# Optimization experiments

Measured on AMD Instinct MI355X. Metric: run time of the kernel, lower is better.

The kernel has to match this reference:

```python
import jax, jax.numpy as jnp
import numpy as np

N = 10000
E = 160000
B = 16
NEG_SLOPE = 0.2


def gat_conv(x, src, dst, W, a_src, a_dst, b, heads, ch):
    # x: [N, F_in]; src/dst: [E'] (self-loops included); W: [F_in, heads*ch]
    n = x.shape[0]
    h = (x @ W).reshape(n, heads, ch)                     # [N,H,C]
    alpha_src = jnp.sum(h * a_src, axis=-1)               # [N,H]
    alpha_dst = jnp.sum(h * a_dst, axis=-1)               # [N,H]
    e = jax.nn.leaky_relu(alpha_src[src] + alpha_dst[dst], NEG_SLOPE)  # [E,H]
    # segment softmax over edges grouped by destination node
    m = jax.ops.segment_max(e, dst, num_segments=n)       # [N,H]
    ex = jnp.exp(e - m[dst])                              # [E,H]
    denom = jax.ops.segment_sum(ex, dst, num_segments=n)  # [N,H]
    alpha = ex / denom[dst]                               # [E,H]
    out = jax.ops.segment_sum(alpha[:, :, None] * h[src], dst, num_segments=n)  # [N,H,C]
    return out.reshape(n, heads * ch) + b


def setup_inputs() -> dict:
    key = jax.random.key(0)
    ks = jax.random.split(key, 16)
    glorot = lambda k, shp: jax.random.normal(k, shp, jnp.float32) * np.sqrt(2.0 / (shp[0] + shp[-1]))
    inp = {
        "x": jax.random.normal(ks[0], (N, 128), jnp.float32),
        "edge_index": jax.random.randint(ks[1], (2, E), 0, N, jnp.int64),
        "batch": jnp.sort(jax.random.randint(ks[2], (N,), 0, B, jnp.int64)),
        # conv1: 128 -> 128 per head, 8 heads
        "W1": glorot(ks[3], (128, 8 * 128)),
        "att_src1": glorot(ks[4], (8, 128)),
        "att_dst1": glorot(ks[5], (8, 128)),
        "b1": jnp.zeros((8 * 128,), jnp.float32),
        # conv2: 1024 -> 64 per head, 8 heads
        "W2": glorot(ks[6], (1024, 8 * 64)),
        "att_src2": glorot(ks[7], (8, 64)),
        "att_dst2": glorot(ks[8], (8, 64)),
        "b2": jnp.zeros((8 * 64,), jnp.float32),
        "fc1_w": glorot(ks[9], (512, 32)),
        "fc1_b": jnp.zeros((32,), jnp.float32),
        "fc2_w": glorot(ks[10], (32, 10)),
        "fc2_b": jnp.zeros((10,), jnp.float32),
    }
    return inp


def reference(x, edge_index, batch, W1, att_src1, att_dst1, b1,
              W2, att_src2, att_dst2, b2, fc1_w, fc1_b, fc2_w, fc2_b):
    n = x.shape[0]
    loop = jnp.arange(n, dtype=edge_index.dtype)
    src = jnp.concatenate([edge_index[0], loop])  # PyG add_self_loops=True
    dst = jnp.concatenate([edge_index[1], loop])
    h = jax.nn.elu(gat_conv(x, src, dst, W1, att_src1, att_dst1, b1, 8, 128))   # [N,1024]
    h = jax.nn.elu(gat_conv(h, src, dst, W2, att_src2, att_dst2, b2, 8, 64))    # [N,512]
    # global mean pool over graphs
    sums = jax.ops.segment_sum(h, batch, num_segments=B)                        # [B,512]
    cnt = jax.ops.segment_sum(jnp.ones((n,), h.dtype), batch, num_segments=B)
    g = sums / jnp.maximum(cnt, 1.0)[:, None]
    g = jax.nn.elu(g @ fc1_w + fc1_b)
    return g @ fc2_w + fc2_b                                                    # [B,10]
```

## Files before the change

kernel.cpp:

```cpp
#include <hip/hip_runtime.h>
#include <math.h>

#define HEADS 8
#define NEG 0.2f

typedef unsigned short ushort_t;
typedef __attribute__((ext_vector_type(8))) short short8;
typedef float f32x4 __attribute__((ext_vector_type(4)));

__device__ inline ushort_t f2bf(float f) {
  union { float f; unsigned u; } v; v.f = f;
  unsigned r = (v.u + 0x7FFF + ((v.u >> 16) & 1)) >> 16;
  return (ushort_t)r;
}

__device__ inline float4 bf4(uint2 v) {
  union { unsigned u; float f; } a, b, c, d;
  a.u = v.x << 16; b.u = v.x & 0xffff0000u;
  c.u = v.y << 16; d.u = v.y & 0xffff0000u;
  return make_float4(a.f, b.f, c.f, d.f);
}

__device__ inline float elu_f(float v) {
  return (v > 0.f) ? v : (__expf(v) - 1.f);
}

#define GLDS16(gp, lp)                                                          \
  __builtin_amdgcn_global_load_lds(                                             \
      (const __attribute__((address_space(1))) void*)(gp),                      \
      (__attribute__((address_space(3))) void*)(lp), 16, 0, 0)

__global__ __launch_bounds__(256) void init_k(int* __restrict__ ws, int zero_words,
                                              const float* __restrict__ x,
                                              ushort_t* __restrict__ xb,
                                              const float* __restrict__ W1,
                                              ushort_t* __restrict__ w1t,
                                              const float* __restrict__ W2,
                                              ushort_t* __restrict__ w2t, int nx4) {
  __shared__ float tile[32][33];
  int blk = blockIdx.x;
  if (blk < 640) {
    const float* W; ushort_t* Wt; int K, N, tk, tn;
    if (blk < 128) { W = W1; Wt = w1t; K = 128; N = 1024; tk = blk >> 5; tn = blk & 31; }
    else { W = W2; Wt = w2t; K = 1024; N = 512; int t = blk - 128; tk = t >> 4; tn = t & 15; }
    int tx = threadIdx.x & 31, ty = threadIdx.x >> 5;
    int k0 = tk * 32, n0 = tn * 32;
#pragma unroll
    for (int r = 0; r < 4; r++)
      tile[ty + r * 8][tx] = W[(size_t)(k0 + ty + r * 8) * N + n0 + tx];
    __syncthreads();
#pragma unroll
    for (int r = 0; r < 4; r++)
      Wt[(size_t)(n0 + ty + r * 8) * K + k0 + tx] = f2bf(tile[tx][ty + r * 8]);
  } else {
    int i = (blk - 640) * 256 + threadIdx.x;
    if (i < zero_words) ws[i] = 0;
    if (i < nx4) {
      float4 v = ((const float4*)x)[i];
      ushort_t o[4] = {f2bf(v.x), f2bf(v.y), f2bf(v.z), f2bf(v.w)};
      *(uint2*)&xb[i * 4] = *(uint2*)o;
    }
  }
}

__global__ void prep_k(const int* __restrict__ ei, int* __restrict__ src,
                       int* __restrict__ dst, int* __restrict__ deg,
                       const int* __restrict__ batch, int* __restrict__ bstart,
                       int* __restrict__ bend, int E, int Nn) {
  int i = blockIdx.x * blockDim.x + threadIdx.x;
  if (i < Nn) {
    int b = batch[i];
    if (i == 0 || batch[i - 1] != b) bstart[b] = i;
    if (i == Nn - 1 || batch[i + 1] != b) bend[b] = i + 1;
  }
  if (i >= E + Nn) return;
  int s, d;
  if (i < E) { s = ei[i]; d = ei[E + i]; }
  else       { s = d = i - E; }
  src[i] = s;
  dst[i] = d;
  atomicAdd(&deg[d], 1);
}

__global__ __launch_bounds__(1024) void scan_k(const int* __restrict__ deg,
                                               int* __restrict__ offs,
                                               int* __restrict__ cursor, int Nn) {
  __shared__ int wtot[16];
  __shared__ int wexcl[16];
  __shared__ int soff_s;
  int t = threadIdx.x;
  int lane = t & 63, w = t >> 6;
  if (t == 0) soff_s = 0;
  __syncthreads();
  for (int base = 0; base < Nn; base += 4096) {
    int idx = base + 4 * t;
    int4 v = make_int4(0, 0, 0, 0);
    if (idx + 3 < Nn) v = *(const int4*)&deg[idx];
    else {
      if (idx < Nn)     v.x = deg[idx];
      if (idx + 1 < Nn) v.y = deg[idx + 1];
      if (idx + 2 < Nn) v.z = deg[idx + 2];
      if (idx + 3 < Nn) v.w = deg[idx + 3];
    }
    int s1 = v.x, s2 = s1 + v.y, s3 = s2 + v.z, s4 = s3 + v.w;
    int sc = s4;
#pragma unroll
    for (int o = 1; o < 64; o <<= 1) {
      int x = __shfl_up(sc, o);
      if (lane >= o) sc += x;
    }
    if (lane == 63) wtot[w] = sc;
    __syncthreads();
    if (w == 0) {
      int tv = (lane < 16) ? wtot[lane] : 0;
      int ts = tv;
#pragma unroll
      for (int o = 1; o < 16; o <<= 1) {
        int x = __shfl_up(ts, o);
        if (lane >= o) ts += x;
      }
      if (lane < 16) wexcl[lane] = ts - tv;
      if (lane == 15) wtot[15] = ts;
    }
    __syncthreads();
    int excl = soff_s + wexcl[w] + (sc - s4);
    int o0 = excl, o1 = excl + s1, o2 = excl + s2, o3 = excl + s3;
    if (idx < Nn)     { offs[idx] = o0;     cursor[idx] = o0; }
    if (idx + 1 < Nn) { offs[idx + 1] = o1; cursor[idx + 1] = o1; }
    if (idx + 2 < Nn) { offs[idx + 2] = o2; cursor[idx + 2] = o2; }
    if (idx + 3 < Nn) { offs[idx + 3] = o3; cursor[idx + 3] = o3; }
    int chunk_total = wtot[15];
    __syncthreads();
    if (t == 0) soff_s += chunk_total;
    __syncthreads();
  }
  if (t == 0) offs[Nn] = soff_s;
}

__global__ void scatter_k(const int* __restrict__ src, const int* __restrict__ dst,
                          int* __restrict__ cursor, int* __restrict__ psrc, int Etot) {
  int i = blockIdx.x * blockDim.x + threadIdx.x;
  if (i >= Etot) return;
  int p = atomicAdd(&cursor[dst[i]], 1);
  psrc[p] = src[i];
}

__global__ __launch_bounds__(256) void mfma_gemm_k(const ushort_t* __restrict__ A,
                                                   const ushort_t* __restrict__ Bt,
                                                   ushort_t* __restrict__ Cb,
                                                   const float* __restrict__ att_s,
                                                   const float* __restrict__ att_d,
                                                   float* __restrict__ asrc,
                                                   float* __restrict__ adst,
                                                   int M, int N, int K, int CSHIFT) {
  __shared__ __attribute__((aligned(16))) ushort_t lds[32768];
  int tid = threadIdx.x;
  int lane = tid & 63;
  int wave = tid >> 6;
  int wm = (wave >> 1) * 64, wn = (wave & 1) * 64;
  int bm = blockIdx.y * 128, bn = blockIdx.x * 128;
  int lrow = lane & 15, lq = lane >> 4;

  f32x4 acc[4][4];
#pragma unroll
  for (int i = 0; i < 4; i++)
#pragma unroll
    for (int j = 0; j < 4; j++) acc[i][j] = 0.f;

  int srow = lane >> 3;
  int scol = 8 * ((lane & 7) ^ srow);
  const ushort_t* pa[4];
  const ushort_t* pb[4];
  int lofs[4];
#pragma unroll
  for (int c = 0; c < 4; c++) {
    int row = wave * 32 + c * 8 + srow;
    int ga = min(bm + row, M - 1);
    pa[c] = &A[(size_t)ga * K + scol];
    pb[c] = &Bt[(size_t)(bn + row) * K + scol];
    lofs[c] = (wave * 4 + c) * 512;
  }

  auto stage = [&](int buf, int k0) {
#pragma unroll
    for (int c = 0; c < 4; c++) GLDS16(pa[c] + k0, &lds[buf * 8192 + lofs[c]]);
#pragma unroll
    for (int c = 0; c < 4; c++) GLDS16(pb[c] + k0, &lds[16384 + buf * 8192 + lofs[c]]);
  };

  auto compute = [&](int buf) {
    const ushort_t* Asb = &lds[buf * 8192];
    const ushort_t* Bsb = &lds[16384 + buf * 8192];
#pragma unroll
    for (int ks = 0; ks < 2; ks++) {
      short8 af[4], bfr[4];
#pragma unroll
      for (int t = 0; t < 4; t++) {
        int cbs = (ks * 64 + lq * 16) ^ ((lrow & 7) << 4);
        af[t]  = *(const short8*)&Asb[(wm + t * 16 + lrow) * 64 + (cbs >> 1)];
        bfr[t] = *(const short8*)&Bsb[(wn + t * 16 + lrow) * 64 + (cbs >> 1)];
      }
#pragma unroll
      for (int i = 0; i < 4; i++)
#pragma unroll
        for (int j = 0; j < 4; j++)
          acc[i][j] = __builtin_amdgcn_mfma_f32_16x16x32_bf16(af[i], bfr[j], acc[i][j], 0, 0, 0);
    }
  };

  int NT = K >> 6;
  stage(0, 0);
  asm volatile("s_waitcnt vmcnt(0)" ::: "memory");
  __builtin_amdgcn_s_barrier();
  int cur = 0;
  for (int t = 0; t + 1 < NT; ++t) {
    stage(cur ^ 1, (t + 1) << 6);
    compute(cur);
    asm volatile("s_waitcnt vmcnt(0)" ::: "memory");
    __builtin_amdgcn_s_barrier();
    cur ^= 1;
  }
  compute(cur);

  __syncthreads();

  ushort_t* Cl = lds;
  float* pls = (float*)&lds[17472];
  float* pld = pls + 256;

  {
    float avs[4], avd[4];
#pragma unroll
    for (int j = 0; j < 4; j++) {
      int col = bn + wn + j * 16 + lrow;
      avs[j] = att_s[col];
      avd[j] = att_d[col];
    }
#pragma unroll
    for (int i = 0; i < 4; i++) {
#pragma unroll
      for (int r = 0; r < 4; r++) {
        float ps = 0.f, pd = 0.f;
#pragma unroll
        for (int j = 0; j < 4; j++) {
          float v = acc[i][j][r];
          ps += v * avs[j];
          pd += v * avd[j];
        }
#pragma unroll
        for (int o = 1; o < 16; o <<= 1) {
          ps += __shfl_xor(ps, o);
          pd += __shfl_xor(pd, o);
        }
        if (lrow == 0) {
          int rr = i * 16 + lq * 4 + r;
          pls[wave * 64 + rr] = ps;
          pld[wave * 64 + rr] = pd;
        }
      }
    }
  }

#pragma unroll
  for (int i = 0; i < 4; i++) {
#pragma unroll
    for (int j = 0; j < 4; j++) {
      int col = wn + j * 16 + lrow;
#pragma unroll
      for (int r = 0; r < 4; r++) {
        int row = wm + i * 16 + lq * 4 + r;
        Cl[row * 136 + col] = f2bf(acc[i][j][r]);
      }
    }
  }
  __syncthreads();

#pragma unroll
  for (int p = 0; p < 8; p++) {
    int row = p * 16 + (tid >> 4);
    int col8 = (tid & 15) * 8;
    if (bm + row < M)
      *(uint4*)&Cb[(size_t)(bm + row) * N + bn + col8] = *(const uint4*)&Cl[row * 136 + col8];
  }

  {
    int r = tid & 127, half = tid >> 7;
    if (bm + r < M) {
      const float* P = half ? pld : pls;
      float* O = half ? adst : asrc;
      int w0 = (r >> 6) * 2, idx = r & 63;
      float va = P[w0 * 64 + idx];
      float vb = P[(w0 + 1) * 64 + idx];
      int h0 = bn >> CSHIFT, h1 = (bn + 64) >> CSHIFT;
      size_t base = (size_t)(bm + r) * HEADS;
      if (h0 == h1) O[base + h0] = va + vb;
      else { O[base + h0] = va; O[base + h1] = vb; }
    }
  }
}

template <int F, int CSHIFT, int BT, int NSPLIT, typename OT>
__global__ __launch_bounds__(BT) void aggregate_k(const ushort_t* __restrict__ hb,
                                                  const float* __restrict__ asrc,
                                                  const float* __restrict__ adst,
                                                  const int* __restrict__ offs,
                                                  const int* __restrict__ psrc,
                                                  const float* __restrict__ bias,
                                                  OT* __restrict__ out) {
  constexpr int CPB = F / NSPLIT;
  constexpr int G = (1 << CSHIFT) >> 2;
  static_assert(CPB == 4 * BT, "CPB/thread mismatch");
  static_assert(G >= 8 && G <= 64, "head group must cover the 8-edge batch");
  int nb = blockIdx.x;
  int n = nb / NSPLIT;
  int coff = (nb - n * NSPLIT) * CPB;
  int t = threadIdx.x;
  int c0 = coff + 4 * t;
  int hh = c0 >> CSHIFT;
  int lane = t & 63;
  int sub = lane & (G - 1);
  int gb = lane & ~(G - 1);
  float adn = adst[n * HEADS + hh];
  int e0 = offs[n], e1 = offs[n + 1];
  float4 acc = make_float4(0.f, 0.f, 0.f, 0.f);
  float wsum = 0.f;

  int i = e0;
  uint2 rA[8];
  float myWA = 0.f;
  bool haveA = (i + 8 <= e1);
  if (haveA) {
    int sA[8];
#pragma unroll
    for (int u = 0; u < 8; u++) sA[u] = psrc[i + u];
#pragma unroll
    for (int u = 0; u < 8; u++) rA[u] = *(const uint2*)&hb[(size_t)sA[u] * F + c0];
    int ms = psrc[i + (sub < 8 ? sub : 0)];
    float v = asrc[ms * HEADS + hh] + adn;
    v = (v > 0.f) ? v : NEG * v;
    myWA = __expf(v);
  }
  while (i + 16 <= e1) {
    int sB[8];
    uint2 rB[8];
#pragma unroll
    for (int u = 0; u < 8; u++) sB[u] = psrc[i + 8 + u];
#pragma unroll
    for (int u = 0; u < 8; u++) rB[u] = *(const uint2*)&hb[(size_t)sB[u] * F + c0];
    int ms = psrc[i + 8 + (sub < 8 ? sub : 0)];
    float vb = asrc[ms * HEADS + hh] + adn;
    vb = (vb > 0.f) ? vb : NEG * vb;
    float myWB = __expf(vb);
#pragma unroll
    for (int u = 0; u < 8; u++) {
      float w = __shfl(myWA, gb + u);
      float4 f = bf4(rA[u]);
      wsum += w;
      acc.x += w * f.x;
      acc.y += w * f.y;
      acc.z += w * f.z;
      acc.w += w * f.w;
    }
    i += 8;
#pragma unroll
    for (int u = 0; u < 8; u++) rA[u] = rB[u];
    myWA = myWB;
  }
  if (haveA) {
#pragma unroll
    for (int u = 0; u < 8; u++) {
      float w = __shfl(myWA, gb + u);
      float4 f = bf4(rA[u]);
      wsum += w;
      acc.x += w * f.x;
      acc.y += w * f.y;
      acc.z += w * f.z;
      acc.w += w * f.w;
    }
    i += 8;
  }
  for (; i < e1; i++) {
    int ss = psrc[i];
    float v = asrc[ss * HEADS + hh] + adn;
    v = (v > 0.f) ? v : NEG * v;
    float w = __expf(v);
    float4 f = bf4(*(const uint2*)&hb[(size_t)ss * F + c0]);
    wsum += w;
    acc.x += w * f.x; acc.y += w * f.y;
    acc.z += w * f.z; acc.w += w * f.w;
  }

  float inv = 1.f / wsum;
  float v0 = elu_f(acc.x * inv + bias[c0]);
  float v1 = elu_f(acc.y * inv + bias[c0 + 1]);
  float v2 = elu_f(acc.z * inv + bias[c0 + 2]);
  float v3 = elu_f(acc.w * inv + bias[c0 + 3]);
  if constexpr (sizeof(OT) == 2) {
    unsigned p0 = (unsigned)f2bf(v0) | ((unsigned)f2bf(v1) << 16);
    unsigned p1 = (unsigned)f2bf(v2) | ((unsigned)f2bf(v3) << 16);
    *(uint2*)&((ushort_t*)out)[(size_t)n * F + c0] = make_uint2(p0, p1);
  } else {
    *(float4*)&((float*)out)[(size_t)n * F + c0] = make_float4(v0, v1, v2, v3);
  }
}

__global__ __launch_bounds__(256) void pool_k(const float* __restrict__ g,
                                              const int* __restrict__ batch,
                                              float* __restrict__ sums, int Nn) {
  int c = blockIdx.x * 256 + threadIdx.x;
  int n0 = blockIdx.y * 50;
  int n1 = min(n0 + 50, Nn);
  if (n0 >= n1) return;
  float acc = 0.f;
  int cur = batch[n0];
  for (int n = n0; n < n1; n++) {
    int b = batch[n];
    if (b != cur) { atomicAdd(&sums[cur * 512 + c], acc); acc = 0.f; cur = b; }
    acc += g[(size_t)n * 512 + c];
  }
  atomicAdd(&sums[cur * 512 + c], acc);
}

__global__ __launch_bounds__(512) void mlp_k(const float* __restrict__ sums,
                                             const int* __restrict__ bstart,
                                             const int* __restrict__ bend,
                                             const float* __restrict__ w1,
                                             const float* __restrict__ b1,
                                             const float* __restrict__ w2,
                                             const float* __restrict__ b2,
                                             float* __restrict__ out) {
  __shared__ float gm[16 * 512];
  __shared__ float t1[16 * 32];
  int t = threadIdx.x;
  for (int i = t; i < 16 * 512; i += 512) {
    int b = i >> 9;
    float c = (float)(bend[b] - bstart[b]);
    gm[i] = sums[i] / fmaxf(c, 1.f);
  }
  __syncthreads();
  {
    int b = t >> 5, j = t & 31;
    float s = b1[j];
    for (int k = 0; k < 512; k++) s += gm[(b << 9) + k] * w1[k * 32 + j];
    t1[t] = elu_f(s);
  }
  __syncthreads();
  if (t < 160) {
    int b = t / 10, j = t - b * 10;
    float s = b2[j];
#pragma unroll
    for (int k = 0; k < 32; k++) s += t1[b * 32 + k] * w2[k * 10 + j];
    out[t] = s;
  }
}

extern "C" void kernel_launch(void* const* d_in, const int* in_sizes, int n_in,
                              void* d_out, int out_size, void* d_ws, size_t ws_size,
                              hipStream_t stream) {
  const float* x   = (const float*)d_in[0];
  const int*   ei  = (const int*)d_in[1];
  const int* batch = (const int*)d_in[2];
  const float* W1  = (const float*)d_in[3];
  const float* as1 = (const float*)d_in[4];
  const float* ad1 = (const float*)d_in[5];
  const float* b1  = (const float*)d_in[6];
  const float* W2  = (const float*)d_in[7];
  const float* as2 = (const float*)d_in[8];
  const float* ad2 = (const float*)d_in[9];
  const float* b2  = (const float*)d_in[10];
  const float* f1w = (const float*)d_in[11];
  const float* f1b = (const float*)d_in[12];
  const float* f2w = (const float*)d_in[13];
  const float* f2b = (const float*)d_in[14];
  float* out = (float*)d_out;

  const int Nn = in_sizes[2];
  const int E = in_sizes[1] / 2;
  const int Etot = E + Nn;

  size_t off = 0;
  auto alloc = [&](size_t elems) { size_t o = off; off += (elems + 63) & ~(size_t)63; return o; };
  int* wsi = (int*)d_ws;
  float* wsf = (float*)d_ws;

  size_t o_deg  = alloc(Nn);
  size_t o_pool = alloc(16 * 512);
  size_t zero_words = off;
  size_t o_as1  = alloc((size_t)Nn * 8);
  size_t o_ad1  = alloc((size_t)Nn * 8);
  size_t o_as2  = alloc((size_t)Nn * 8);
  size_t o_ad2  = alloc((size_t)Nn * 8);
  size_t o_bst  = alloc(64);
  size_t o_ben  = alloc(64);
  size_t o_offs = alloc(Nn + 1);
  size_t o_cur  = alloc(Nn);
  size_t o_src  = alloc(Etot);
  size_t o_dst  = alloc(Etot);
  size_t o_psrc = alloc(Etot);
  size_t o_xb   = alloc((size_t)Nn * 128 / 2);
  size_t o_w1t  = alloc(1024 * 128 / 2);
  size_t o_w2t  = alloc(512 * 1024 / 2);
  size_t o_h    = alloc((size_t)Nn * 1024 / 2);
  size_t o_g    = alloc((size_t)Nn * 1024);

  ushort_t* xb  = (ushort_t*)(wsi + o_xb);
  ushort_t* w1t = (ushort_t*)(wsi + o_w1t);
  ushort_t* w2t = (ushort_t*)(wsi + o_w2t);
  ushort_t* hb  = (ushort_t*)(wsi + o_h);
  ushort_t* g1b = (ushort_t*)(wsi + o_g);

  int eb = (Etot + 255) / 256;

  int nx4 = Nn * 128 / 4;
  int ep_work = (int)((zero_words > (size_t)nx4 ? zero_words : (size_t)nx4));
  int init_blocks = 640 + (ep_work + 255) / 256;
  init_k<<<init_blocks, 256, 0, stream>>>(wsi, (int)zero_words, x, xb,
                                          W1, w1t, W2, w2t, nx4);
  prep_k<<<eb, 256, 0, stream>>>(ei, wsi + o_src, wsi + o_dst, wsi + o_deg,
                                 batch, wsi + o_bst, wsi + o_ben, E, Nn);
  scan_k<<<1, 1024, 0, stream>>>(wsi + o_deg, wsi + o_offs, wsi + o_cur, Nn);
  scatter_k<<<eb, 256, 0, stream>>>(wsi + o_src, wsi + o_dst, wsi + o_cur,
                                    wsi + o_psrc, Etot);

  mfma_gemm_k<<<dim3(1024 / 128, (Nn + 127) / 128), 256, 0, stream>>>(
      xb, w1t, hb, as1, ad1, wsf + o_as1, wsf + o_ad1, Nn, 1024, 128, 7);
  aggregate_k<1024, 7, 128, 2, ushort_t><<<Nn * 2, 128, 0, stream>>>(
      hb, wsf + o_as1, wsf + o_ad1, wsi + o_offs, wsi + o_psrc, b1, g1b);

  mfma_gemm_k<<<dim3(512 / 128, (Nn + 127) / 128), 256, 0, stream>>>(
      g1b, w2t, hb, as2, ad2, wsf + o_as2, wsf + o_ad2, Nn, 512, 1024, 6);
  aggregate_k<512, 6, 64, 2, float><<<Nn * 2, 64, 0, stream>>>(
      hb, wsf + o_as2, wsf + o_ad2, wsi + o_offs, wsi + o_psrc, b2, wsf + o_g);

  pool_k<<<dim3(2, (Nn + 49) / 50), 256, 0, stream>>>(wsf + o_g, batch, wsf + o_pool, Nn);
  mlp_k<<<1, 512, 0, stream>>>(wsf + o_pool, wsi + o_bst, wsi + o_ben, f1w, f1b, f2w, f2b, out);
}
```

Measured before the change: 254.9 us.

## Aggregate raw features before projection in first GAT layer

Layer 1 now uses linearity: the attention logits are computed as x·(W1·a) through a small precomputed projection, and the softmax-weighted sum runs over the 128-wide bf16 input features for each head instead of the 1024-wide projected features. A per-head GEMM then multiplies the aggregated [N,8,128] features by that head's W1 slice and fuses bias and ELU. The gather traffic per edge shrinks from 1024 to 128 values, at the cost of an extra intermediate buffer, several new kernels, and slightly different rounding.

```diff
diff --git a/kernel.cpp b/kernel.cpp
--- a/kernel.cpp
+++ b/kernel.cpp
@@ -145,6 +145,209 @@
   psrc[p] = src[i];
 }
 
+__global__ __launch_bounds__(256) void pa_k(const float* __restrict__ W1,
+                                            const float* __restrict__ as1,
+                                            const float* __restrict__ ad1,
+                                            float* __restrict__ Ps,
+                                            float* __restrict__ Pd) {
+  int h = blockIdx.x;
+  int t = threadIdx.x;
+  int k = t >> 1, sd = t & 1;
+  const float* att = sd ? ad1 : as1;
+  float* P = sd ? Pd : Ps;
+  const float* wrow = &W1[(size_t)k * 1024 + h * 128];
+  const float* arow = &att[h * 128];
+  float s = 0.f;
+#pragma unroll 8
+  for (int c = 0; c < 128; c++) s += wrow[c] * arow[c];
+  P[k * 8 + h] = s;
+}
+
+__global__ __launch_bounds__(256) void al1_k(const float* __restrict__ x,
+                                             const float* __restrict__ Ps,
+                                             const float* __restrict__ Pd,
+                                             float* __restrict__ asrc,
+                                             float* __restrict__ adst, int Nn) {
+  __shared__ float ps[1024], pd[1024];
+  int t = threadIdx.x;
+  for (int i = t; i < 1024; i += 256) { ps[i] = Ps[i]; pd[i] = Pd[i]; }
+  __syncthreads();
+  int n = blockIdx.x * 256 + t;
+  if (n >= Nn) return;
+  const float4* xr = (const float4*)&x[(size_t)n * 128];
+  float as[8], ad[8];
+#pragma unroll
+  for (int h = 0; h < 8; h++) { as[h] = 0.f; ad[h] = 0.f; }
+  for (int k4 = 0; k4 < 32; k4++) {
+    float4 xv = xr[k4];
+    float xs[4] = {xv.x, xv.y, xv.z, xv.w};
+#pragma unroll
+    for (int j = 0; j < 4; j++) {
+      int k = k4 * 4 + j;
+#pragma unroll
+      for (int h = 0; h < 8; h++) {
+        as[h] += xs[j] * ps[k * 8 + h];
+        ad[h] += xs[j] * pd[k * 8 + h];
+      }
+    }
+  }
+#pragma unroll
+  for (int h = 0; h < 8; h++) {
+    asrc[n * 8 + h] = as[h];
+    adst[n * 8 + h] = ad[h];
+  }
+}
+
+__global__ __launch_bounds__(64) void aggx_k(const ushort_t* __restrict__ xb,
+                                             const float* __restrict__ asrc,
+                                             const float* __restrict__ adst,
+                                             const int* __restrict__ offs,
+                                             const int* __restrict__ psrc,
+                                             ushort_t* __restrict__ sb, int Nn) {
+  int n = blockIdx.x;
+  int l = threadIdx.x;
+  int u_mine = l >> 3, h_mine = l & 7;
+  float adn = adst[n * 8 + h_mine];
+  int e0 = offs[n], e1 = offs[n + 1];
+  int c0 = l * 2;
+  float acc0[8], acc1[8], wsum[8];
+#pragma unroll
+  for (int h = 0; h < 8; h++) { acc0[h] = 0.f; acc1[h] = 0.f; wsum[h] = 0.f; }
+
+  for (int i = e0; i < e1; i += 8) {
+    int bs = min(8, e1 - i);
+    int eu = i + (u_mine < bs ? u_mine : bs - 1);
+    int se = psrc[eu];
+    float v = asrc[se * 8 + h_mine] + adn;
+    v = (v > 0.f) ? v : NEG * v;
+    float wm = __expf(v);
+    int ss[8];
+    unsigned xvv[8];
+#pragma unroll
+    for (int u = 0; u < 8; u++) ss[u] = psrc[i + (u < bs ? u : bs - 1)];
+#pragma unroll
+    for (int u = 0; u < 8; u++) xvv[u] = *(const unsigned*)&xb[(size_t)ss[u] * 128 + c0];
+#pragma unroll
+    for (int u = 0; u < 8; u++) {
+      if (u < bs) {
+        union { unsigned u; float f; } a, b;
+        a.u = xvv[u] << 16; b.u = xvv[u] & 0xffff0000u;
+#pragma unroll
+        for (int h = 0; h < 8; h++) {
+          float w = __shfl(wm, (u << 3) | h);
+          acc0[h] += w * a.f;
+          acc1[h] += w * b.f;
+          wsum[h] += w;
+        }
+      }
+    }
+  }
+
+#pragma unroll
+  for (int h = 0; h < 8; h++) {
+    float inv = 1.f / wsum[h];
+    unsigned pr = (unsigned)f2bf(acc0[h] * inv) | ((unsigned)f2bf(acc1[h] * inv) << 16);
+    *(unsigned*)&sb[(size_t)n * 1024 + h * 128 + c0] = pr;
+  }
+}
+
+__global__ __launch_bounds__(256) void hgemm_k(const ushort_t* __restrict__ S,
+                                               const ushort_t* __restrict__ Wt,
+                                               const float* __restrict__ bias,
+                                               ushort_t* __restrict__ G, int M) {
+  __shared__ __attribute__((aligned(16))) ushort_t lds[32768];
+  int tid = threadIdx.x;
+  int lane = tid & 63;
+  int wave = tid >> 6;
+  int wm = (wave >> 1) * 64, wn = (wave & 1) * 64;
+  int head = blockIdx.x;
+  int hb0 = head * 128;
+  int bm = blockIdx.y * 128;
+  int lrow = lane & 15, lq = lane >> 4;
+
+  f32x4 acc[4][4];
+#pragma unroll
+  for (int i = 0; i < 4; i++)
+#pragma unroll
+    for (int j = 0; j < 4; j++) acc[i][j] = 0.f;
+
+  int srow = lane >> 3;
+  int scol = 8 * ((lane & 7) ^ srow);
+  const ushort_t* pa[4];
+  const ushort_t* pb[4];
+  int lofs[4];
+#pragma unroll
+  for (int c = 0; c < 4; c++) {
+    int row = wave * 32 + c * 8 + srow;
+    int ga = min(bm + row, M - 1);
+    pa[c] = &S[(size_t)ga * 1024 + hb0 + scol];
+    pb[c] = &Wt[(size_t)(hb0 + row) * 128 + scol];
+    lofs[c] = (wave * 4 + c) * 512;
+  }
+
+  auto stage = [&](int buf, int k0) {
+#pragma unroll
+    for (int c = 0; c < 4; c++) GLDS16(pa[c] + k0, &lds[buf * 8192 + lofs[c]]);
+#pragma unroll
+    for (int c = 0; c < 4; c++) GLDS16(pb[c] + k0, &lds[16384 + buf * 8192 + lofs[c]]);
+  };
+  auto compute = [&](int buf) {
+    const ushort_t* Asb = &lds[buf * 8192];
+    const ushort_t* Bsb = &lds[16384 + buf * 8192];
+#pragma unroll
+    for (int ks = 0; ks < 2; ks++) {
+      short8 af[4], bfr[4];
+#pragma unroll
+      for (int t = 0; t < 4; t++) {
+        int cbs = (ks * 64 + lq * 16) ^ ((lrow & 7) << 4);
+        af[t]  = *(const short8*)&Asb[(wm + t * 16 + lrow) * 64 + (cbs >> 1)];
+        bfr[t] = *(const short8*)&Bsb[(wn + t * 16 + lrow) * 64 + (cbs >> 1)];
+      }
+#pragma unroll
+      for (int i = 0; i < 4; i++)
+#pragma unroll
+        for (int j = 0; j < 4; j++)
+          acc[i][j] = __builtin_amdgcn_mfma_f32_16x16x32_bf16(af[i], bfr[j], acc[i][j], 0, 0, 0);
+    }
+  };
+
+  stage(0, 0);
+  asm volatile("s_waitcnt vmcnt(0)" ::: "memory");
+  __builtin_amdgcn_s_barrier();
+  stage(1, 64);
+  compute(0);
+  asm volatile("s_waitcnt vmcnt(0)" ::: "memory");
+  __builtin_amdgcn_s_barrier();
+  compute(1);
+
+  __syncthreads();
+
+  ushort_t* Cl = lds;
+  float bv[4];
+#pragma unroll
+  for (int j = 0; j < 4; j++) bv[j] = bias[hb0 + wn + j * 16 + lrow];
+#pragma unroll
+  for (int i = 0; i < 4; i++) {
+#pragma unroll
+    for (int j = 0; j < 4; j++) {
+      int col = wn + j * 16 + lrow;
+#pragma unroll
+      for (int r = 0; r < 4; r++) {
+        int row = wm + i * 16 + lq * 4 + r;
+        Cl[row * 136 + col] = f2bf(elu_f(acc[i][j][r] + bv[j]));
+      }
+    }
+  }
+  __syncthreads();
+#pragma unroll
+  for (int p = 0; p < 8; p++) {
+    int row = p * 16 + (tid >> 4);
+    int col8 = (tid & 15) * 8;
+    if (bm + row < M)
+      *(uint4*)&G[(size_t)(bm + row) * 1024 + hb0 + col8] = *(const uint4*)&Cl[row * 136 + col8];
+  }
+}
+
 __global__ __launch_bounds__(256) void mfma_gemm_k(const ushort_t* __restrict__ A,
                                                    const ushort_t* __restrict__ Bt,
                                                    ushort_t* __restrict__ Cb,
@@ -187,7 +390,6 @@
 #pragma unroll
     for (int c = 0; c < 4; c++) GLDS16(pb[c] + k0, &lds[16384 + buf * 8192 + lofs[c]]);
   };
-
   auto compute = [&](int buf) {
     const ushort_t* Asb = &lds[buf * 8192];
     const ushort_t* Bsb = &lds[16384 + buf * 8192];
@@ -490,6 +692,8 @@
   size_t o_ad1  = alloc((size_t)Nn * 8);
   size_t o_as2  = alloc((size_t)Nn * 8);
   size_t o_ad2  = alloc((size_t)Nn * 8);
+  size_t o_ps   = alloc(1024);
+  size_t o_pd   = alloc(1024);
   size_t o_bst  = alloc(64);
   size_t o_ben  = alloc(64);
   size_t o_offs = alloc(Nn + 1);
@@ -500,12 +704,14 @@
   size_t o_xb   = alloc((size_t)Nn * 128 / 2);
   size_t o_w1t  = alloc(1024 * 128 / 2);
   size_t o_w2t  = alloc(512 * 1024 / 2);
+  size_t o_s    = alloc((size_t)Nn * 1024 / 2);
   size_t o_h    = alloc((size_t)Nn * 1024 / 2);
   size_t o_g    = alloc((size_t)Nn * 1024);
 
   ushort_t* xb  = (ushort_t*)(wsi + o_xb);
   ushort_t* w1t = (ushort_t*)(wsi + o_w1t);
   ushort_t* w2t = (ushort_t*)(wsi + o_w2t);
+  ushort_t* sb  = (ushort_t*)(wsi + o_s);
   ushort_t* hb  = (ushort_t*)(wsi + o_h);
   ushort_t* g1b = (ushort_t*)(wsi + o_g);
 
@@ -522,10 +728,12 @@
   scatter_k<<<eb, 256, 0, stream>>>(wsi + o_src, wsi + o_dst, wsi + o_cur,
                                     wsi + o_psrc, Etot);
 
-  mfma_gemm_k<<<dim3(1024 / 128, (Nn + 127) / 128), 256, 0, stream>>>(
-      xb, w1t, hb, as1, ad1, wsf + o_as1, wsf + o_ad1, Nn, 1024, 128, 7);
-  aggregate_k<1024, 7, 128, 2, ushort_t><<<Nn * 2, 128, 0, stream>>>(
-      hb, wsf + o_as1, wsf + o_ad1, wsi + o_offs, wsi + o_psrc, b1, g1b);
+  pa_k<<<8, 256, 0, stream>>>(W1, as1, ad1, wsf + o_ps, wsf + o_pd);
+  al1_k<<<(Nn + 255) / 256, 256, 0, stream>>>(x, wsf + o_ps, wsf + o_pd,
+                                              wsf + o_as1, wsf + o_ad1, Nn);
+  aggx_k<<<Nn, 64, 0, stream>>>(xb, wsf + o_as1, wsf + o_ad1,
+                                wsi + o_offs, wsi + o_psrc, sb, Nn);
+  hgemm_k<<<dim3(8, (Nn + 127) / 128), 256, 0, stream>>>(sb, w1t, b1, g1b, Nn);
 
   mfma_gemm_k<<<dim3(512 / 128, (Nn + 127) / 128), 256, 0, stream>>>(
       g1b, w2t, hb, as2, ad2, wsf + o_as2, wsf + o_ad2, Nn, 512, 1024, 6);
```

Result: faster. 249.7 us, median of 2 (-2.0%).
